# Kernel tuning notes

Measured on AMD Instinct MI355X. Metric: run time of the kernel, lower is better.

The kernel has to match this reference:

```python
import jax, jax.numpy as jnp
import numpy as np

N_AGENT = 60000
N_MAP = 40000
N = N_AGENT + N_MAP
E = 3200000
HID = 32
PERIODS = 30
PRED = 50


def setup_inputs() -> dict:
    key = jax.random.key(0)
    ks = jax.random.split(key, 20)
    def w(k, shape, s=0.1):
        return jax.random.normal(k, shape, jnp.float32) * s
    return {
        "agent_x": jax.random.normal(ks[0], (N_AGENT, 9), jnp.float32),
        "map_x": jax.random.normal(ks[1], (N_MAP, 6), jnp.float32),
        "edge_index": jax.random.randint(ks[2], (2, E), 0, N),
        "W_agent": w(ks[3], (9, HID)), "b_agent": jnp.zeros((HID,), jnp.float32),
        "W_map": w(ks[4], (6, HID)), "b_map": jnp.zeros((HID,), jnp.float32),
        # TGCN cell: three GCNConvs (z, r, h gates) + three Linear(2*HID -> HID)
        "Wz_c": w(ks[5], (HID, HID)), "bz_c": jnp.zeros((HID,), jnp.float32),
        "Wr_c": w(ks[6], (HID, HID)), "br_c": jnp.zeros((HID,), jnp.float32),
        "Wh_c": w(ks[7], (HID, HID)), "bh_c": jnp.zeros((HID,), jnp.float32),
        "Wz_l": w(ks[8], (2 * HID, HID)), "bz_l": jnp.zeros((HID,), jnp.float32),
        "Wr_l": w(ks[9], (2 * HID, HID)), "br_l": jnp.zeros((HID,), jnp.float32),
        "Wh_l": w(ks[10], (2 * HID, HID)), "bh_l": jnp.zeros((HID,), jnp.float32),
        "attn": w(ks[11], (PERIODS,), 1.0),
        "W1": w(ks[12], (HID, 2 * HID)), "b1": jnp.zeros((2 * HID,), jnp.float32),
        "W2": w(ks[13], (2 * HID, 2 * PRED)), "b2": jnp.zeros((2 * PRED,), jnp.float32),
    }


def reference(agent_x, map_x, edge_index, W_agent, b_agent, W_map, b_map,
              Wz_c, bz_c, Wr_c, br_c, Wh_c, bh_c,
              Wz_l, bz_l, Wr_l, br_l, Wh_l, bh_l,
              attn, W1, b1, W2, b2):
    n = agent_x.shape[0] + map_x.shape[0]
    # encoders + concat map nodes after agent nodes
    x = jnp.concatenate([agent_x @ W_agent + b_agent,
                         map_x @ W_map + b_map], axis=0)  # [N, HID]

    # GCN normalization with self-loops: A_hat = D^-1/2 (A + I) D^-1/2
    loop = jnp.arange(n, dtype=edge_index.dtype)
    src = jnp.concatenate([edge_index[0], loop])
    dst = jnp.concatenate([edge_index[1], loop])
    deg = jax.ops.segment_sum(jnp.ones(src.shape[0], jnp.float32), dst, num_segments=n)
    dinv = jnp.where(deg > 0, jax.lax.rsqrt(deg), 0.0)
    norm = dinv[src] * dinv[dst]  # [E + N]

    def gcn(W, b):
        m = (x @ W)[src] * norm[:, None]          # gather + scale: [E+N, HID]
        return jax.ops.segment_sum(m, dst, num_segments=n) + b

    zeros_h = jnp.zeros_like(x)  # hidden state H = 0 (A3TGCN never threads H)
    z = jax.nn.sigmoid(jnp.concatenate([gcn(Wz_c, bz_c), zeros_h], 1) @ Wz_l + bz_l)
    r = jax.nn.sigmoid(jnp.concatenate([gcn(Wr_c, br_c), zeros_h], 1) @ Wr_l + br_l)
    h_tilde = jnp.tanh(jnp.concatenate([gcn(Wh_c, bh_c), zeros_h * r], 1) @ Wh_l + bh_l)
    h_new = (1.0 - z) * h_tilde  # z*H + (1-z)*h_tilde with H=0

    # attention-weighted sum over periods; every period is identical so it
    # collapses to sum(softmax(attn)) * h_new (== h_new, kept for fidelity)
    probs = jax.nn.softmax(attn)
    h_acc = jnp.sum(probs) * h_new

    h = jax.nn.relu(h_acc)[:agent_x.shape[0]]     # keep agent nodes only
    pred = jax.nn.relu(h @ W1 + b1) @ W2 + b2     # [num_agents, 2*PRED]
    return pred.reshape(-1, PRED, 2)
```

## Files before the change

### kernel.cpp

```cpp
#include <hip/hip_runtime.h>
#include <math.h>

#define N_AGENT 60000
#define N_MAP   40000
#define N_NODES 100000
#define NE      3200000
#define HID     32
#define PERIODS 30

#define NBUCK   391
#define NABUCK  235
#define CAP     10240
#define TILE    4096
#define PTHREADS 512
#define ABLK    64

__global__ void k_precompute(const float* Wz_c, const float* bz_c,
                             const float* Wh_c, const float* bh_c,
                             const float* Wz_l, const float* bz_l,
                             const float* Wh_l, const float* bh_l,
                             const float* attn,
                             float* Mz, float* Mh, float* bz_eff, float* bh_eff,
                             float* s_out, int* cursor) {
    int t = threadIdx.x;
    int k = t >> 5, c = t & 31;
    float mz = 0.f, mh = 0.f;
    for (int j = 0; j < HID; ++j) {
        mz += Wz_c[k * HID + j] * Wz_l[j * HID + c];
        mh += Wh_c[k * HID + j] * Wh_l[j * HID + c];
    }
    Mz[t] = mz; Mh[t] = mh;
    if (t < NBUCK) cursor[t] = t * CAP;
    if (t < HID) {
        float bz = bz_l[t], bh = bh_l[t];
        for (int j = 0; j < HID; ++j) {
            bz += bz_c[j] * Wz_l[j * HID + t];
            bh += bh_c[j] * Wh_l[j * HID + t];
        }
        bz_eff[t] = bz; bh_eff[t] = bh;
    }
    if (t == 0) {
        float m = -1e30f;
        for (int i = 0; i < PERIODS; ++i) m = fmaxf(m, attn[i]);
        float S = 0.f;
        for (int i = 0; i < PERIODS; ++i) S += expf(attn[i] - m);
        float s = 0.f;
        for (int i = 0; i < PERIODS; ++i) s += expf(attn[i] - m) / S;
        *s_out = s;
    }
}

__global__ __launch_bounds__(PTHREADS) void k_partition(
        const int* __restrict__ src, const int* __restrict__ dst,
        int* __restrict__ cursor, int* __restrict__ ebuf) {
    __shared__ int sCnt[NBUCK + 1];
    __shared__ int sBase[NBUCK + 1];
    __shared__ int sGbase[NBUCK];
    __shared__ int sScan[PTHREADS];
    __shared__ int sReorder[TILE];
    int t = threadIdx.x;
    int tileBase = blockIdx.x * TILE;
    int tcount = NE - tileBase; if (tcount > TILE) tcount = TILE;

    if (t < NBUCK) sCnt[t] = 0;
    __syncthreads();

    int pb[8]; int pp[8];
#pragma unroll
    for (int k = 0; k < 8; ++k) {
        int e = tileBase + t + k * PTHREADS;
        pb[k] = -1;
        if (e < NE) {
            int s = src[e], d = dst[e];
            pb[k] = d >> 8;
            pp[k] = s | ((d & 255) << 17);
            atomicAdd(&sCnt[pb[k]], 1);
        }
    }
    __syncthreads();

    int v = (t < NBUCK) ? sCnt[t] : 0;
    sScan[t] = v;
    __syncthreads();
    for (int s = 1; s < PTHREADS; s <<= 1) {
        int a = (t >= s) ? sScan[t - s] : 0;
        __syncthreads();
        sScan[t] += a;
        __syncthreads();
    }
    if (t <= NBUCK) sBase[t] = sScan[t] - v;
    __syncthreads();
    if (t < NBUCK) {
        if (sCnt[t] > 0) sGbase[t] = atomicAdd(&cursor[t], sCnt[t]);
        sCnt[t] = 0;
    }
    __syncthreads();
#pragma unroll
    for (int k = 0; k < 8; ++k) {
        if (pb[k] >= 0) {
            int r = atomicAdd(&sCnt[pb[k]], 1);
            sReorder[sBase[pb[k]] + r] = pp[k];
        }
    }
    __syncthreads();
#pragma unroll
    for (int k = 0; k < 8; ++k) {
        int j = t + k * PTHREADS;
        if (j < tcount) {
            int lo = 0, hi = NBUCK;
            while (hi - lo > 1) {
                int m = (lo + hi) >> 1;
                if (sBase[m] <= j) lo = m; else hi = m;
            }
            ebuf[sGbase[lo] + (j - sBase[lo])] = sReorder[j];
        }
    }
}

__global__ __launch_bounds__(256) void k_hist(const int* __restrict__ cursor,
                                              const int* __restrict__ ebuf,
                                              int* __restrict__ deg) {
    __shared__ int h[256];
    int t = threadIdx.x;
    int b = blockIdx.x;
    h[t] = 0;
    __syncthreads();
    int start = b * CAP;
    int cnt = cursor[b] - start;
    for (int j = t; j < cnt; j += 256)
        atomicAdd(&h[(ebuf[start + j] >> 17) & 255], 1);
    __syncthreads();
    int node = b * 256 + t;
    if (node < N_NODES) deg[node] = h[t];
}

__global__ void k_encode(const float* __restrict__ agent_x, const float* __restrict__ map_x,
                         const float* __restrict__ W_agent, const float* __restrict__ b_agent,
                         const float* __restrict__ W_map, const float* __restrict__ b_map,
                         const int* __restrict__ deg,
                         float* __restrict__ y) {
    int t = blockIdx.x * blockDim.x + threadIdx.x;
    if (t >= N_NODES * HID) return;
    int i = t >> 5, c = t & 31;
    float acc;
    if (i < N_AGENT) {
        const float* row = agent_x + (size_t)i * 9;
        acc = b_agent[c];
#pragma unroll
        for (int k = 0; k < 9; ++k) acc += row[k] * W_agent[k * HID + c];
    } else {
        const float* row = map_x + (size_t)(i - N_AGENT) * 6;
        acc = b_map[c];
#pragma unroll
        for (int k = 0; k < 6; ++k) acc += row[k] * W_map[k * HID + c];
    }
    float di = rsqrtf((float)deg[i] + 1.0f);
    y[t] = acc * di;
}

__global__ __launch_bounds__(1024) void k_sortlocal(
        const int* __restrict__ cursor, int* __restrict__ ebuf,
        const int* __restrict__ deg, int* __restrict__ row_start) {
    __shared__ int sSorted[CAP];
    __shared__ int sBase[256];
    __shared__ int sCnt[256];
    __shared__ int sScan[256];
    int t = threadIdx.x;
    const int b = blockIdx.x;
    const int nodeBase = b * 256;

    int d0 = 0;
    if (t < 256) {
        d0 = deg[nodeBase + t];
        sCnt[t] = 0;
        sScan[t] = d0;
    }
    __syncthreads();
    for (int st = 1; st < 256; st <<= 1) {
        int a = 0;
        if (t < 256 && t >= st) a = sScan[t - st];
        __syncthreads();
        if (t < 256) sScan[t] += a;
        __syncthreads();
    }
    if (t < 256) {
        sBase[t] = sScan[t] - d0;
        row_start[nodeBase + t] = b * CAP + sBase[t];
    }
    __syncthreads();

    const int start = b * CAP;
    const int cnt = cursor[b] - start;
    for (int j = t; j < cnt; j += 1024) {
        int p = ebuf[start + j];
        int dl = (p >> 17) & 255;
        int r = atomicAdd(&sCnt[dl], 1);
        sSorted[sBase[dl] + r] = p & 0x1FFFF;
    }
    __syncthreads();
    for (int j = t; j < cnt; j += 1024)
        ebuf[start + j] = sSorted[j];
}

__global__ __launch_bounds__(1024) void k_aggmlp(
        const int* __restrict__ row_start, const int* __restrict__ deg,
        const int* __restrict__ ebuf, const float* __restrict__ y,
        const float* __restrict__ Mz, const float* __restrict__ Mh,
        const float* __restrict__ bz_eff, const float* __restrict__ bh_eff,
        const float* __restrict__ s_ptr,
        const float* __restrict__ W1, const float* __restrict__ b1,
        const float* __restrict__ W2, const float* __restrict__ b2,
        float* __restrict__ out) {
    __shared__ float sAcc[ABLK * 32];
    __shared__ float sMz[1024], sMh[1024], sW1[2048], sW2[6400];
    __shared__ float sbz[32], sbh[32], sb1[64], sb2[100];
    int t = threadIdx.x;
    sMz[t] = Mz[t]; sMh[t] = Mh[t];
    for (int j = t; j < 2048; j += 1024) sW1[j] = W1[j];
    for (int j = t; j < 6400; j += 1024) sW2[j] = W2[j];
    if (t < 32) { sbz[t] = bz_eff[t]; sbh[t] = bh_eff[t]; }
    if (t >= 32 && t < 96) sb1[t - 32] = b1[t - 32];
    if (t >= 128 && t < 228) sb2[t - 128] = b2[t - 128];

    const int nodeBase = blockIdx.x * ABLK;
    const int w = t >> 6, lane = t & 63;
    const int g = lane >> 3, q = lane & 7;
    const float4* y4 = (const float4*)y;

#pragma unroll
    for (int k = 0; k < 4; ++k) {
        int r = w * 4 + k;
        int i = nodeBase + r;
        if (i >= N_AGENT) break;
        int e0 = row_start[i];
        int e1 = e0 + deg[i];
        float ax = 0.f, ay = 0.f, az = 0.f, aw = 0.f;
        int j = e0 + g;
        for (; j + 24 < e1; j += 32) {
            int s0 = ebuf[j];
            int s1 = ebuf[j + 8];
            int s2 = ebuf[j + 16];
            int s3 = ebuf[j + 24];
            float4 v0 = y4[(size_t)s0 * 8 + q];
            float4 v1 = y4[(size_t)s1 * 8 + q];
            float4 v2 = y4[(size_t)s2 * 8 + q];
            float4 v3 = y4[(size_t)s3 * 8 + q];
            ax += (v0.x + v1.x) + (v2.x + v3.x);
            ay += (v0.y + v1.y) + (v2.y + v3.y);
            az += (v0.z + v1.z) + (v2.z + v3.z);
            aw += (v0.w + v1.w) + (v2.w + v3.w);
        }
        for (; j < e1; j += 8) {
            int s0 = ebuf[j];
            float4 v0 = y4[(size_t)s0 * 8 + q];
            ax += v0.x; ay += v0.y; az += v0.z; aw += v0.w;
        }
#pragma unroll
        for (int off = 8; off <= 32; off <<= 1) {
            ax += __shfl_xor(ax, off, 64);
            ay += __shfl_xor(ay, off, 64);
            az += __shfl_xor(az, off, 64);
            aw += __shfl_xor(aw, off, 64);
        }
        if (g == 0)
            *(float4*)&sAcc[r * 32 + q * 4] = make_float4(ax, ay, az, aw);
    }
    __syncthreads();

    const float s = *s_ptr;
    const int c = t & 31, g2 = t >> 5;
    for (int r = g2; r < ABLK; r += 32) {
        int i = nodeBase + r;
        if (i >= N_AGENT) break;
        float di = rsqrtf((float)deg[i] + 1.0f);
        float a = (sAcc[r * 32 + c] + y[(size_t)i * HID + c]) * di;
        float uz = sbz[c], uh = sbh[c];
#pragma unroll
        for (int k = 0; k < 32; ++k) {
            float ak = __shfl(a, k, 32);
            uz += ak * sMz[k * 32 + c];
            uh += ak * sMh[k * 32 + c];
        }
        float z = 1.0f / (1.0f + expf(-uz));
        float h = s * (1.0f - z) * tanhf(uh);
        h = fmaxf(h, 0.0f);
        float t0 = sb1[c], t1 = sb1[c + 32];
#pragma unroll
        for (int k = 0; k < 32; ++k) {
            float hk = __shfl(h, k, 32);
            t0 += hk * sW1[k * 64 + c];
            t1 += hk * sW1[k * 64 + c + 32];
        }
        t0 = fmaxf(t0, 0.0f); t1 = fmaxf(t1, 0.0f);
        int j3 = (c < 4) ? (c + 96) : 99;
        float o0 = sb2[c];
        float o1 = sb2[c + 32];
        float o2 = sb2[c + 64];
        float o3 = sb2[j3];
#pragma unroll
        for (int k = 0; k < 32; ++k) {
            float ta = __shfl(t0, k, 32);
            float tb = __shfl(t1, k, 32);
            o0 += ta * sW2[k * 100 + c]      + tb * sW2[(k + 32) * 100 + c];
            o1 += ta * sW2[k * 100 + c + 32] + tb * sW2[(k + 32) * 100 + c + 32];
            o2 += ta * sW2[k * 100 + c + 64] + tb * sW2[(k + 32) * 100 + c + 64];
            o3 += ta * sW2[k * 100 + j3]     + tb * sW2[(k + 32) * 100 + j3];
        }
        float* orow = out + (size_t)i * 100;
        orow[c] = o0;
        orow[c + 32] = o1;
        orow[c + 64] = o2;
        if (c < 4) orow[c + 96] = o3;
    }
}

extern "C" void kernel_launch(void* const* d_in, const int* in_sizes, int n_in,
                              void* d_out, int out_size, void* d_ws, size_t ws_size,
                              hipStream_t stream) {
    const float* agent_x = (const float*)d_in[0];
    const float* map_x   = (const float*)d_in[1];
    const int*   ei      = (const int*)d_in[2];
    const float* W_agent = (const float*)d_in[3];
    const float* b_agent = (const float*)d_in[4];
    const float* W_map   = (const float*)d_in[5];
    const float* b_map   = (const float*)d_in[6];
    const float* Wz_c    = (const float*)d_in[7];
    const float* bz_c    = (const float*)d_in[8];
    const float* Wh_c    = (const float*)d_in[11];
    const float* bh_c    = (const float*)d_in[12];
    const float* Wz_l    = (const float*)d_in[13];
    const float* bz_l    = (const float*)d_in[14];
    const float* Wh_l    = (const float*)d_in[17];
    const float* bh_l    = (const float*)d_in[18];
    const float* attn    = (const float*)d_in[19];
    const float* W1      = (const float*)d_in[20];
    const float* b1      = (const float*)d_in[21];
    const float* W2      = (const float*)d_in[22];
    const float* b2      = (const float*)d_in[23];
    float* out = (float*)d_out;

    const int* e_src = ei;
    const int* e_dst = ei + NE;

    float* ws       = (float*)d_ws;
    float* y        = ws;
    float* Mz       = ws + 3200000;
    float* Mh       = ws + 3201024;
    float* bz       = ws + 3202048;
    float* bh       = ws + 3202080;
    float* sS       = ws + 3202112;
    int*   deg      = (int*)(ws + 3202304);
    int*   cursor   = (int*)(ws + 3302400);
    int*   row_start= (int*)(ws + 3302912);
    int*   ebuf     = (int*)(ws + 3363328);

    k_precompute<<<1, 1024, 0, stream>>>(Wz_c, bz_c, Wh_c, bh_c, Wz_l, bz_l,
                                         Wh_l, bh_l, attn, Mz, Mh, bz, bh, sS, cursor);
    k_partition<<<(NE + TILE - 1) / TILE, PTHREADS, 0, stream>>>(e_src, e_dst, cursor, ebuf);
    k_hist<<<NBUCK, 256, 0, stream>>>(cursor, ebuf, deg);
    k_encode<<<(N_NODES * HID + 255) / 256, 256, 0, stream>>>(
        agent_x, map_x, W_agent, b_agent, W_map, b_map, deg, y);
    k_sortlocal<<<NABUCK, 1024, 0, stream>>>(cursor, ebuf, deg, row_start);
    k_aggmlp<<<(N_AGENT + ABLK - 1) / ABLK, 1024, 0, stream>>>(
        row_start, deg, ebuf, y, Mz, Mh, bz, bh, sS, W1, b1, W2, b2, out);
}
```

Before: 349.0 us.

## Vectorize partition loads, reuse rank atomics, stage edge lists in LDS for aggregation

The partition kernel now reads src/dst as int4 and keeps the rank returned by the first shared-memory atomic, so the second atomic pass is gone. The encoder loads each input row once per warp and broadcasts it with shuffles. It also writes a zero padding row at index N_NODES. The aggregation kernel stages each block's contiguous edge slice into shared memory and pads tail loads with the zero row, removing the scalar remainder loop, with a global-memory fallback when the slice exceeds the buffer. Workspace offsets shift to make room for the padding row.

```diff
diff --git a/kernel.cpp b/kernel.cpp
--- a/kernel.cpp
+++ b/kernel.cpp
@@ -14,6 +14,7 @@
 #define TILE    4096
 #define PTHREADS 512
 #define ABLK    64
+#define EBLK    4096
 
 __global__ void k_precompute(const float* Wz_c, const float* bz_c,
                              const float* Wh_c, const float* bh_c,
@@ -53,7 +54,7 @@
 __global__ __launch_bounds__(PTHREADS) void k_partition(
         const int* __restrict__ src, const int* __restrict__ dst,
         int* __restrict__ cursor, int* __restrict__ ebuf) {
-    __shared__ int sCnt[NBUCK + 1];
+    __shared__ int sCnt[NBUCK];
     __shared__ int sBase[NBUCK + 1];
     __shared__ int sGbase[NBUCK];
     __shared__ int sScan[PTHREADS];
@@ -65,17 +66,25 @@
     if (t < NBUCK) sCnt[t] = 0;
     __syncthreads();
 
-    int pb[8]; int pp[8];
-#pragma unroll
-    for (int k = 0; k < 8; ++k) {
-        int e = tileBase + t + k * PTHREADS;
-        pb[k] = -1;
-        if (e < NE) {
-            int s = src[e], d = dst[e];
-            pb[k] = d >> 8;
-            pp[k] = s | ((d & 255) << 17);
-            atomicAdd(&sCnt[pb[k]], 1);
-        }
+    int pb[8], pp[8], pr[8];
+    const int4* s4 = (const int4*)src;
+    const int4* d4 = (const int4*)dst;
+#pragma unroll
+    for (int k = 0; k < 2; ++k) {
+        int e4 = (tileBase >> 2) + t + k * PTHREADS;
+        int valid = (e4 << 2) < NE;
+        int4 sv, dv;
+        if (valid) { sv = s4[e4]; dv = d4[e4]; }
+#define PROC(m, SS, DD) { int kk = k * 4 + m;                                  \
+        if (valid) { pb[kk] = (DD) >> 8;                                       \
+                     pp[kk] = (SS) | (((DD) & 255) << 17);                     \
+                     pr[kk] = atomicAdd(&sCnt[pb[kk]], 1); }                   \
+        else pb[kk] = -1; }
+        PROC(0, sv.x, dv.x)
+        PROC(1, sv.y, dv.y)
+        PROC(2, sv.z, dv.z)
+        PROC(3, sv.w, dv.w)
+#undef PROC
     }
     __syncthreads();
 
@@ -90,17 +99,11 @@
     }
     if (t <= NBUCK) sBase[t] = sScan[t] - v;
     __syncthreads();
-    if (t < NBUCK) {
-        if (sCnt[t] > 0) sGbase[t] = atomicAdd(&cursor[t], sCnt[t]);
-        sCnt[t] = 0;
-    }
+    if (t < NBUCK && sCnt[t] > 0) sGbase[t] = atomicAdd(&cursor[t], sCnt[t]);
     __syncthreads();
 #pragma unroll
     for (int k = 0; k < 8; ++k) {
-        if (pb[k] >= 0) {
-            int r = atomicAdd(&sCnt[pb[k]], 1);
-            sReorder[sBase[pb[k]] + r] = pp[k];
-        }
+        if (pb[k] >= 0) sReorder[sBase[pb[k]] + pr[k]] = pp[k];
     }
     __syncthreads();
 #pragma unroll
@@ -140,22 +143,23 @@
                          const int* __restrict__ deg,
                          float* __restrict__ y) {
     int t = blockIdx.x * blockDim.x + threadIdx.x;
-    if (t >= N_NODES * HID) return;
+    if (t >= (N_NODES + 1) * HID) return;
     int i = t >> 5, c = t & 31;
-    float acc;
+    float acc = 0.f;
     if (i < N_AGENT) {
-        const float* row = agent_x + (size_t)i * 9;
+        float v = (c < 9) ? agent_x[(size_t)i * 9 + c] : 0.f;
         acc = b_agent[c];
 #pragma unroll
-        for (int k = 0; k < 9; ++k) acc += row[k] * W_agent[k * HID + c];
-    } else {
-        const float* row = map_x + (size_t)(i - N_AGENT) * 6;
+        for (int k = 0; k < 9; ++k) acc += __shfl(v, k, 32) * W_agent[k * HID + c];
+        acc *= rsqrtf((float)deg[i] + 1.0f);
+    } else if (i < N_NODES) {
+        float v = (c < 6) ? map_x[(size_t)(i - N_AGENT) * 6 + c] : 0.f;
         acc = b_map[c];
 #pragma unroll
-        for (int k = 0; k < 6; ++k) acc += row[k] * W_map[k * HID + c];
-    }
-    float di = rsqrtf((float)deg[i] + 1.0f);
-    y[t] = acc * di;
+        for (int k = 0; k < 6; ++k) acc += __shfl(v, k, 32) * W_map[k * HID + c];
+        acc *= rsqrtf((float)deg[i] + 1.0f);
+    }
+    y[t] = acc;
 }
 
 __global__ __launch_bounds__(1024) void k_sortlocal(
@@ -211,59 +215,106 @@
         const float* __restrict__ W1, const float* __restrict__ b1,
         const float* __restrict__ W2, const float* __restrict__ b2,
         float* __restrict__ out) {
+    __shared__ int   sEdge[EBLK];
+    __shared__ int   sOff[ABLK + 1];
     __shared__ float sAcc[ABLK * 32];
     __shared__ float sMz[1024], sMh[1024], sW1[2048], sW2[6400];
     __shared__ float sbz[32], sbh[32], sb1[64], sb2[100];
     int t = threadIdx.x;
+    const int nodeBase = blockIdx.x * ABLK;
+
     sMz[t] = Mz[t]; sMh[t] = Mh[t];
     for (int j = t; j < 2048; j += 1024) sW1[j] = W1[j];
     for (int j = t; j < 6400; j += 1024) sW2[j] = W2[j];
     if (t < 32) { sbz[t] = bz_eff[t]; sbh[t] = bh_eff[t]; }
     if (t >= 32 && t < 96) sb1[t - 32] = b1[t - 32];
     if (t >= 128 && t < 228) sb2[t - 128] = b2[t - 128];
-
-    const int nodeBase = blockIdx.x * ABLK;
+    if (t < ABLK) sOff[t] = row_start[nodeBase + t];
+    if (t == ABLK) {
+        int last = nodeBase + ABLK - 1;
+        sOff[ABLK] = row_start[last] + deg[last];
+    }
+    __syncthreads();
+
+    const int e_begin = sOff[0];
+    const int cnt = sOff[ABLK] - e_begin;
+    for (int j = t; j < cnt && j < EBLK; j += 1024) sEdge[j] = ebuf[e_begin + j];
+    __syncthreads();
+
     const int w = t >> 6, lane = t & 63;
     const int g = lane >> 3, q = lane & 7;
     const float4* y4 = (const float4*)y;
 
-#pragma unroll
-    for (int k = 0; k < 4; ++k) {
-        int r = w * 4 + k;
-        int i = nodeBase + r;
-        if (i >= N_AGENT) break;
-        int e0 = row_start[i];
-        int e1 = e0 + deg[i];
-        float ax = 0.f, ay = 0.f, az = 0.f, aw = 0.f;
-        int j = e0 + g;
-        for (; j + 24 < e1; j += 32) {
-            int s0 = ebuf[j];
-            int s1 = ebuf[j + 8];
-            int s2 = ebuf[j + 16];
-            int s3 = ebuf[j + 24];
-            float4 v0 = y4[(size_t)s0 * 8 + q];
-            float4 v1 = y4[(size_t)s1 * 8 + q];
-            float4 v2 = y4[(size_t)s2 * 8 + q];
-            float4 v3 = y4[(size_t)s3 * 8 + q];
-            ax += (v0.x + v1.x) + (v2.x + v3.x);
-            ay += (v0.y + v1.y) + (v2.y + v3.y);
-            az += (v0.z + v1.z) + (v2.z + v3.z);
-            aw += (v0.w + v1.w) + (v2.w + v3.w);
-        }
-        for (; j < e1; j += 8) {
-            int s0 = ebuf[j];
-            float4 v0 = y4[(size_t)s0 * 8 + q];
-            ax += v0.x; ay += v0.y; az += v0.z; aw += v0.w;
-        }
-#pragma unroll
-        for (int off = 8; off <= 32; off <<= 1) {
-            ax += __shfl_xor(ax, off, 64);
-            ay += __shfl_xor(ay, off, 64);
-            az += __shfl_xor(az, off, 64);
-            aw += __shfl_xor(aw, off, 64);
-        }
-        if (g == 0)
-            *(float4*)&sAcc[r * 32 + q * 4] = make_float4(ax, ay, az, aw);
+    if (cnt <= EBLK) {
+#pragma unroll
+        for (int k = 0; k < 4; ++k) {
+            int r = w * 4 + k;
+            int i = nodeBase + r;
+            if (i >= N_AGENT) break;
+            int e0 = sOff[r] - e_begin, e1 = sOff[r + 1] - e_begin;
+            float ax = 0.f, ay = 0.f, az = 0.f, aw = 0.f;
+            for (int j = e0 + g; j < e1; j += 32) {
+                int i0 = sEdge[j];
+                int i1 = (j + 8  < e1) ? sEdge[j + 8]  : N_NODES;
+                int i2 = (j + 16 < e1) ? sEdge[j + 16] : N_NODES;
+                int i3 = (j + 24 < e1) ? sEdge[j + 24] : N_NODES;
+                float4 v0 = y4[(size_t)i0 * 8 + q];
+                float4 v1 = y4[(size_t)i1 * 8 + q];
+                float4 v2 = y4[(size_t)i2 * 8 + q];
+                float4 v3 = y4[(size_t)i3 * 8 + q];
+                ax += (v0.x + v1.x) + (v2.x + v3.x);
+                ay += (v0.y + v1.y) + (v2.y + v3.y);
+                az += (v0.z + v1.z) + (v2.z + v3.z);
+                aw += (v0.w + v1.w) + (v2.w + v3.w);
+            }
+#pragma unroll
+            for (int off = 8; off <= 32; off <<= 1) {
+                ax += __shfl_xor(ax, off, 64);
+                ay += __shfl_xor(ay, off, 64);
+                az += __shfl_xor(az, off, 64);
+                aw += __shfl_xor(aw, off, 64);
+            }
+            if (g == 0)
+                *(float4*)&sAcc[r * 32 + q * 4] = make_float4(ax, ay, az, aw);
+        }
+    } else {
+#pragma unroll
+        for (int k = 0; k < 4; ++k) {
+            int r = w * 4 + k;
+            int i = nodeBase + r;
+            if (i >= N_AGENT) break;
+            int e0 = sOff[r], e1 = sOff[r + 1];
+            float ax = 0.f, ay = 0.f, az = 0.f, aw = 0.f;
+            int j = e0 + g;
+            for (; j + 24 < e1; j += 32) {
+                int s0 = ebuf[j];
+                int s1 = ebuf[j + 8];
+                int s2 = ebuf[j + 16];
+                int s3 = ebuf[j + 24];
+                float4 v0 = y4[(size_t)s0 * 8 + q];
+                float4 v1 = y4[(size_t)s1 * 8 + q];
+                float4 v2 = y4[(size_t)s2 * 8 + q];
+                float4 v3 = y4[(size_t)s3 * 8 + q];
+                ax += (v0.x + v1.x) + (v2.x + v3.x);
+                ay += (v0.y + v1.y) + (v2.y + v3.y);
+                az += (v0.z + v1.z) + (v2.z + v3.z);
+                aw += (v0.w + v1.w) + (v2.w + v3.w);
+            }
+            for (; j < e1; j += 8) {
+                int s0 = ebuf[j];
+                float4 v0 = y4[(size_t)s0 * 8 + q];
+                ax += v0.x; ay += v0.y; az += v0.z; aw += v0.w;
+            }
+#pragma unroll
+            for (int off = 8; off <= 32; off <<= 1) {
+                ax += __shfl_xor(ax, off, 64);
+                ay += __shfl_xor(ay, off, 64);
+                az += __shfl_xor(az, off, 64);
+                aw += __shfl_xor(aw, off, 64);
+            }
+            if (g == 0)
+                *(float4*)&sAcc[r * 32 + q * 4] = make_float4(ax, ay, az, aw);
+        }
     }
     __syncthreads();
 
@@ -344,21 +395,21 @@
 
     float* ws       = (float*)d_ws;
     float* y        = ws;
-    float* Mz       = ws + 3200000;
-    float* Mh       = ws + 3201024;
-    float* bz       = ws + 3202048;
-    float* bh       = ws + 3202080;
-    float* sS       = ws + 3202112;
-    int*   deg      = (int*)(ws + 3202304);
-    int*   cursor   = (int*)(ws + 3302400);
-    int*   row_start= (int*)(ws + 3302912);
+    float* Mz       = ws + 3200256;
+    float* Mh       = ws + 3201280;
+    float* bz       = ws + 3202304;
+    float* bh       = ws + 3202336;
+    float* sS       = ws + 3202368;
+    int*   deg      = (int*)(ws + 3202560);
+    int*   cursor   = (int*)(ws + 3302656);
+    int*   row_start= (int*)(ws + 3303168);
     int*   ebuf     = (int*)(ws + 3363328);
 
     k_precompute<<<1, 1024, 0, stream>>>(Wz_c, bz_c, Wh_c, bh_c, Wz_l, bz_l,
                                          Wh_l, bh_l, attn, Mz, Mh, bz, bh, sS, cursor);
     k_partition<<<(NE + TILE - 1) / TILE, PTHREADS, 0, stream>>>(e_src, e_dst, cursor, ebuf);
     k_hist<<<NBUCK, 256, 0, stream>>>(cursor, ebuf, deg);
-    k_encode<<<(N_NODES * HID + 255) / 256, 256, 0, stream>>>(
+    k_encode<<<((N_NODES + 1) * HID + 255) / 256, 256, 0, stream>>>(
         agent_x, map_x, W_agent, b_agent, W_map, b_map, deg, y);
     k_sortlocal<<<NABUCK, 1024, 0, stream>>>(cursor, ebuf, deg, row_start);
     k_aggmlp<<<(N_AGENT + ABLK - 1) / ABLK, 1024, 0, stream>>>(
```

New measurement: 332.1 us. 1.05x faster.
